# Performance work log

Measured on AMD Instinct MI355X. Metric: run time of the kernel, lower is better.

Reference implementation:

```python
import jax, jax.numpy as jnp
import numpy as np

B, D_IN, H, D_OUT = 1024, 512, 512, 512


def _act(v):
    # torch.relu(x) ** 2
    r = jnp.maximum(v, 0.0)
    return r * r


def setup_inputs() -> dict:
    key = jax.random.key(0)
    ks = jax.random.split(key, 8)
    x = jax.random.normal(ks[0], (B, D_IN), dtype=jnp.float32)
    # input_to_hidden: Linear(D_IN, H)
    W_in = jax.random.normal(ks[1], (D_IN, H), dtype=jnp.float32) / np.sqrt(D_IN)
    b_in = jax.random.normal(ks[2], (H,), dtype=jnp.float32) * 0.01
    # hidden_to_hidden[i]: Linear(1, H-i-1). Pack into padded arrays [H-1, H]
    # where row i, column j is the weight feeding output index j (valid only j > i).
    W_hh = jax.random.normal(ks[3], (H - 1, H), dtype=jnp.float32) * 0.02
    b_hh = jax.random.normal(ks[4], (H - 1, H), dtype=jnp.float32) * 0.01
    # hidden_to_output: Linear(H, D_OUT)
    W_out = jax.random.normal(ks[5], (H, D_OUT), dtype=jnp.float32) / np.sqrt(H)
    b_out = jax.random.normal(ks[6], (D_OUT,), dtype=jnp.float32) * 0.01
    return {"x": x, "W_in": W_in, "b_in": b_in, "W_hh": W_hh, "b_hh": b_hh,
            "W_out": W_out, "b_out": b_out}


def reference(x, W_in, b_in, W_hh, b_hh, W_out, b_out):
    h0 = _act(x @ W_in + b_in)  # [B, H]
    hid = h0.shape[1]
    col = jnp.arange(hid)

    def step(h, inp):
        i, w, b = inp  # w, b: [H] padded rows
        src = jnp.take(h, i, axis=1)  # [B], uses UPDATED h (strict sequential dep)
        contrib = _act(src[:, None] * w[None, :] + b[None, :])  # [B, H]
        mask = (col > i).astype(h.dtype)  # only columns i+1.. get updated
        return h + contrib * mask[None, :], None

    xs = (jnp.arange(hid - 1), W_hh, b_hh)
    h, _ = jax.lax.scan(step, h0, xs)
    return h @ W_out + b_out  # [B, D_OUT]
```

## Files before the change

kernel.cpp:

```cpp
#include <hip/hip_runtime.h>

#define B_SZ 1024
#define DIN 512
#define HH 512
#define DOUT 512

typedef short bf16x8 __attribute__((ext_vector_type(8)));
typedef float f32x4 __attribute__((ext_vector_type(4)));

__device__ __forceinline__ unsigned short f2bf(float f) {
    unsigned int u = __float_as_uint(f);
    u += 0x7FFFu + ((u >> 16) & 1u);
    return (unsigned short)(u >> 16);
}
__device__ __forceinline__ float bf2f(unsigned short s) {
    return __uint_as_float(((unsigned int)s) << 16);
}

__device__ __forceinline__ uint4 cvt8(const float4& a0, const float4& a1, int term) {
    const float av[8] = {a0.x, a0.y, a0.z, a0.w, a1.x, a1.y, a1.z, a1.w};
    unsigned int p[4];
    #pragma unroll
    for (int q = 0; q < 4; ++q) {
        float f0 = av[2 * q], f1 = av[2 * q + 1];
        unsigned short h0 = f2bf(f0), h1 = f2bf(f1);
        if (term == 1) { h0 = f2bf(f0 - bf2f(h0)); h1 = f2bf(f1 - bf2f(h1)); }
        p[q] = (unsigned int)h0 | ((unsigned int)h1 << 16);
    }
    uint4 v; v.x = p[0]; v.y = p[1]; v.z = p[2]; v.w = p[3];
    return v;
}

__device__ __forceinline__ void gload_lds16(const void* g, void* l) {
    __builtin_amdgcn_global_load_lds(
        (__attribute__((address_space(1))) void*)g,
        (__attribute__((address_space(3))) void*)l, 16, 0, 0);
}

template <int N>
__device__ __forceinline__ void waitcnt_vm() {
    asm volatile("s_waitcnt vmcnt(%0)" :: "n"(N) : "memory");
}

__device__ __forceinline__ void convW_body(const float* __restrict__ W,
                                           uint4* __restrict__ dst, int t) {
    const int lane = t & 63;
    const int fb   = t >> 6;
    const int ks   = fb >> 5;
    const int nf   = fb & 31;
    const int col  = nf * 16 + (lane & 15);
    const int kb   = ks * 32 + ((lane >> 4) << 3);
    const int term = kb >> 9;
    const int c0   = kb & 511;
    unsigned short o[8];
    #pragma unroll
    for (int j = 0; j < 8; ++j) {
        const float f = W[(size_t)(c0 + j) * 512 + col];
        unsigned short hi = f2bf(f);
        o[j] = (term == 2) ? f2bf(f - bf2f(hi)) : hi;
    }
    uint4 v;
    v.x = (unsigned int)o[0] | ((unsigned int)o[1] << 16);
    v.y = (unsigned int)o[2] | ((unsigned int)o[3] << 16);
    v.z = (unsigned int)o[4] | ((unsigned int)o[5] << 16);
    v.w = (unsigned int)o[6] | ((unsigned int)o[7] << 16);
    dst[t] = v;
}

template <int C>
__device__ __forceinline__ void pack_bulk(const float* __restrict__ W_hh,
                                          const float* __restrict__ b_hh,
                                          float2* __restrict__ wbk, int e) {
    constexpr int NK = 7 - C;
    constexpr int CB = (C==0?0:C==1?7:C==2?13:C==3?18:C==4?22:C==5?25:27) * 4096;
    const int s   = e / (NK * 64);
    const int rem = e - s * (NK * 64);
    const int row = 64 * C + s;
    const int col = 64 * (C + 1) + rem;
    float2 o;
    o.x = W_hh[(size_t)row * 512 + col];
    o.y = b_hh[(size_t)row * 512 + col];
    wbk[CB + e] = o;
}

__global__ __launch_bounds__(256)
void prep_all(const float* __restrict__ W_hh, const float* __restrict__ b_hh,
              float2* __restrict__ wdg, float2* __restrict__ wbk,
              const float* __restrict__ W_in, uint4* __restrict__ Bin,
              const float* __restrict__ W_out, uint4* __restrict__ Bout) {
    const int b = blockIdx.x;
    const int tid = threadIdx.x;
    if (b < 128) {
        const int idx = b * 256 + tid;
        const int i = idx >> 6, l = idx & 63;
        float2 o;
        if (i < 511 && l > (i & 63)) {
            const int col = ((i >> 6) << 6) + l;
            o.x = W_hh[(size_t)i * 512 + col];
            o.y = b_hh[(size_t)i * 512 + col];
        } else { o.x = 0.0f; o.y = -1.0f; }
        wdg[idx] = o;
    } else if (b < 576) {
        const int rb = b - 128;
        if      (rb < 112) pack_bulk<0>(W_hh, b_hh, wbk, (rb      ) * 256 + tid);
        else if (rb < 208) pack_bulk<1>(W_hh, b_hh, wbk, (rb - 112) * 256 + tid);
        else if (rb < 288) pack_bulk<2>(W_hh, b_hh, wbk, (rb - 208) * 256 + tid);
        else if (rb < 352) pack_bulk<3>(W_hh, b_hh, wbk, (rb - 288) * 256 + tid);
        else if (rb < 400) pack_bulk<4>(W_hh, b_hh, wbk, (rb - 352) * 256 + tid);
        else if (rb < 432) pack_bulk<5>(W_hh, b_hh, wbk, (rb - 400) * 256 + tid);
        else               pack_bulk<6>(W_hh, b_hh, wbk, (rb - 432) * 256 + tid);
    } else if (b < 960) {
        convW_body(W_in, Bin, (b - 576) * 256 + tid);
    } else {
        convW_body(W_out, Bout, (b - 960) * 256 + tid);
    }
}

template <bool ACT>
__global__ __launch_bounds__(512, 2)
void mfma_gemm(const float* __restrict__ A,
               const uint4* __restrict__ Bg,
               const float* __restrict__ bias,
               float* __restrict__ C) {
    __shared__ uint4 lds[2][768];
    const int tid  = threadIdx.x;
    const int lane = tid & 63;
    const int w    = tid >> 6;
    const int mfw  = w & 3;
    const int nfw  = w >> 2;
    const int mf0  = blockIdx.x * 4;
    const int nf0  = blockIdx.y * 2;

    const int ks_s = tid >> 8;
    const int mf_s = (tid >> 6) & 3;
    const int arow = (mf0 + mf_s) * 16 + (lane & 15);
    const int koff = (lane >> 4) << 3;
    const int bks  = tid >> 7;
    const int bnf  = (tid >> 6) & 1;

    float4 Ra0, Ra1; uint4 R2;
    auto stage = [&](int s) {
        const int kp = (s * 2 + ks_s) * 32 + koff;
        const int c  = kp & 511;
        Ra0 = *(const float4*)&A[(size_t)arow * 512 + c];
        Ra1 = *(const float4*)&A[(size_t)arow * 512 + c + 4];
        if (tid < 256)
            R2 = Bg[(size_t)((s * 2 + bks) * 32 + nf0 + bnf) * 64 + lane];
    };
    auto write_tile = [&](int buf, int s) {
        const int kp = (s * 2 + ks_s) * 32 + koff;
        lds[buf][ks_s * 256 + mf_s * 64 + lane] = cvt8(Ra0, Ra1, kp >> 9);
        if (tid < 256)
            lds[buf][512 + bks * 128 + bnf * 64 + lane] = R2;
    };

    f32x4 acc = {0.f, 0.f, 0.f, 0.f};

    stage(0);
    write_tile(0, 0);
    stage(1);
    __syncthreads();

    for (int s = 0; s < 24; ++s) {
        const int cur = s & 1;
        if (s + 1 < 24) write_tile(cur ^ 1, s + 1);
        if (s + 2 < 24) stage(s + 2);
        __builtin_amdgcn_sched_barrier(0);

        bf16x8 aF0 = *(const bf16x8*)&lds[cur][          mfw * 64 + lane];
        bf16x8 aF1 = *(const bf16x8*)&lds[cur][256     + mfw * 64 + lane];
        bf16x8 bF0 = *(const bf16x8*)&lds[cur][512     + nfw * 64 + lane];
        bf16x8 bF1 = *(const bf16x8*)&lds[cur][512+128 + nfw * 64 + lane];
        acc = __builtin_amdgcn_mfma_f32_16x16x32_bf16(aF0, bF0, acc, 0, 0, 0);
        acc = __builtin_amdgcn_mfma_f32_16x16x32_bf16(aF1, bF1, acc, 0, 0, 0);
        __syncthreads();
    }

    const int colg  = (nf0 + nfw) * 16 + (lane & 15);
    const float bv  = bias[colg];
    const int rbase = (mf0 + mfw) * 16 + ((lane >> 4) << 2);
    #pragma unroll
    for (int r = 0; r < 4; ++r) {
        float v = acc[r] + bv;
        if (ACT) { v = fmaxf(v, 0.f); v = v * v; }
        C[(size_t)(rbase + r) * 512 + colg] = v;
    }
}

template <int C>
__device__ __forceinline__ void scan_chunk(const float2* __restrict__ wdg,
                                           const float2* __restrict__ wbk,
                                           float2 (* __restrict__ smb)[3584],
                                           float hr[8], int lane, int tid) {
    constexpr int NK = 7 - C;
    constexpr int CB = (C==0?0:C==1?7:C==2?13:C==3?18:C==4?22:C==5?25:C==6?27:27) * 4096;
    const float2* dptr = wdg + (64 * C) * 64 + lane;

    const char* gch = (const char*)(wbk + CB);
    char* lbase = (char*)(&smb[0][0]) + ((tid >> 6) << 10);
    auto stage = [&](int t, int buf) {
        const char* g = gch + (size_t)t * (NK * 4096);
        char* l = lbase + buf * 28672;
        #pragma unroll
        for (int u = 0; u < NK; ++u)
            gload_lds16(g + (size_t)((u << 8) + tid) * 16, l + (u << 12));
    };
    if constexpr (NK > 0) { stage(0, 0); stage(1, 1); }
    __builtin_amdgcn_sched_barrier(0);

    float2 Wd[16];
    #pragma unroll
    for (int q = 0; q < 16; ++q) Wd[q] = dptr[q * 64];

    for (int t = 0; t < 4; ++t) {
        #pragma unroll
        for (int q = 0; q < 16; ++q) {
            const int s = t * 16 + q;
            if (!(C == 7 && s == 63)) {
                const float hi = __uint_as_float(
                    __builtin_amdgcn_readlane(__float_as_uint(hr[C]), s));
                const float tv = fmaf(hi, Wd[q].x, Wd[q].y);
                const float rv = fmaxf(tv, 0.f);
                hr[C] = fmaf(rv, rv, hr[C]);
            }
            if (t < 3) Wd[q] = dptr[(s + 16) * 64];
        }
    }

    if constexpr (NK > 0) {
        #pragma unroll
        for (int t = 0; t < 8; ++t) {
            if (t + 2 < 8) stage(t + 2, (t + 2) & 3);
            __builtin_amdgcn_sched_barrier(0);
            if      (t <= 5) waitcnt_vm<2 * NK>();
            else if (t == 6) waitcnt_vm<NK>();
            else             waitcnt_vm<0>();
            __builtin_amdgcn_s_barrier();
            __builtin_amdgcn_sched_barrier(0);

            #pragma unroll 2
            for (int s = 0; s < 8; ++s) {
                const float hi = __uint_as_float(
                    __builtin_amdgcn_readlane(__float_as_uint(hr[C]), t * 8 + s));
                #pragma unroll
                for (int k = 0; k < NK; ++k) {
                    const float2 wv = smb[t & 3][(s * NK + k) * 64 + lane];
                    const float tv = fmaf(hi, wv.x, wv.y);
                    const float rv = fmaxf(tv, 0.f);
                    hr[C + 1 + k] = fmaf(rv, rv, hr[C + 1 + k]);
                }
            }
        }
    }
}

__global__ __launch_bounds__(256, 1)
void scan_kernel(const float2* __restrict__ wdg, const float2* __restrict__ wbk,
                 float* __restrict__ h) {
    __shared__ __align__(16) float2 smb[4][3584];
    const int tid  = threadIdx.x;
    const int lane = tid & 63;
    const int wave = tid >> 6;
    const int row  = blockIdx.x * 4 + wave;
    float* hrow = h + (size_t)row * HH;

    float hr[8];
    #pragma unroll
    for (int k = 0; k < 8; ++k) hr[k] = hrow[lane + 64 * k];

    scan_chunk<0>(wdg, wbk, smb, hr, lane, tid);
    scan_chunk<1>(wdg, wbk, smb, hr, lane, tid);
    scan_chunk<2>(wdg, wbk, smb, hr, lane, tid);
    scan_chunk<3>(wdg, wbk, smb, hr, lane, tid);
    scan_chunk<4>(wdg, wbk, smb, hr, lane, tid);
    scan_chunk<5>(wdg, wbk, smb, hr, lane, tid);
    scan_chunk<6>(wdg, wbk, smb, hr, lane, tid);
    scan_chunk<7>(wdg, wbk, smb, hr, lane, tid);

    #pragma unroll
    for (int k = 0; k < 8; ++k) hrow[lane + 64 * k] = hr[k];
}

extern "C" void kernel_launch(void* const* d_in, const int* in_sizes, int n_in,
                              void* d_out, int out_size, void* d_ws, size_t ws_size,
                              hipStream_t stream) {
    const float* x     = (const float*)d_in[0];
    const float* W_in  = (const float*)d_in[1];
    const float* b_in  = (const float*)d_in[2];
    const float* W_hh  = (const float*)d_in[3];
    const float* b_hh  = (const float*)d_in[4];
    const float* W_out = (const float*)d_in[5];
    const float* b_out = (const float*)d_in[6];
    float* out = (float*)d_out;

    char* ws = (char*)d_ws;
    float2* wdg  = (float2*)ws;
    float2* wbk  = (float2*)(ws + 0x040000u);
    float*  h    = (float*)(ws + 0x120000u);
    uint4*  Bin  = (uint4*)(ws + 0x320000u);
    uint4*  Bout = (uint4*)(ws + 0x4A0000u);

    prep_all<<<dim3(1344), dim3(256), 0, stream>>>(W_hh, b_hh, wdg, wbk,
                                                   W_in, Bin, W_out, Bout);

    mfma_gemm<true><<<dim3(16, 16), dim3(512), 0, stream>>>(x, Bin, b_in, h);

    scan_kernel<<<dim3(256), dim3(256), 0, stream>>>(wdg, wbk, h);

    mfma_gemm<false><<<dim3(16, 16), dim3(512), 0, stream>>>(h, Bout, b_out, out);
}
```

Measured before the change: 160.5 us.

## Split each scan row across two waves sharing hidden columns via LDS

The scan kernel now uses 512 threads per block, so each batch row is handled by two waves that own interleaved 64-column chunks of the hidden state. The wave owning the current diagonal chunk runs the sequential inner scan and publishes its chunk through a small shared buffer. Both waves then apply the bulk updates for their own columns, which halves per-wave register state and bulk work and doubles wave count. The cost is an extra block-wide barrier per chunk, plus the non-owner wave sitting idle during the serial diagonal phase.

```diff
diff --git a/kernel.cpp b/kernel.cpp
--- a/kernel.cpp
+++ b/kernel.cpp
@@ -187,14 +187,35 @@
     }
 }
 
+template <int C, int H>
+__device__ __forceinline__ void bulk_half(const float2* __restrict__ tile,
+                                          const float his[8], float hrl[4],
+                                          int lane) {
+    constexpr int NK = 7 - C;
+    constexpr int I0 = (C + 2 - H) >> 1;
+    #pragma unroll
+    for (int s = 0; s < 8; ++s) {
+        #pragma unroll
+        for (int i = I0; i < 4; ++i) {
+            const float2 wv = tile[(s * NK + (2 * i + H - C - 1)) * 64 + lane];
+            const float tv = fmaf(his[s], wv.x, wv.y);
+            const float rv = fmaxf(tv, 0.f);
+            hrl[i] = fmaf(rv, rv, hrl[i]);
+        }
+    }
+}
+
 template <int C>
 __device__ __forceinline__ void scan_chunk(const float2* __restrict__ wdg,
                                            const float2* __restrict__ wbk,
                                            float2 (* __restrict__ smb)[3584],
-                                           float hr[8], int lane, int tid) {
+                                           float (* __restrict__ comm)[64],
+                                           float hrl[4], int lane, int half,
+                                           int r, int tid) {
     constexpr int NK = 7 - C;
     constexpr int CB = (C==0?0:C==1?7:C==2?13:C==3?18:C==4?22:C==5?25:C==6?27:27) * 4096;
-    const float2* dptr = wdg + (64 * C) * 64 + lane;
+    constexpr int IO = C >> 1;
+    const bool owner = (half == (C & 1));
 
     const char* gch = (const char*)(wbk + CB);
     char* lbase = (char*)(&smb[0][0]) + ((tid >> 6) << 10);
@@ -205,32 +226,40 @@
         for (int u = 0; u < NK; ++u)
             gload_lds16(g + (size_t)((u << 8) + tid) * 16, l + (u << 12));
     };
-    if constexpr (NK > 0) { stage(0, 0); stage(1, 1); }
+    if constexpr (NK > 0) {
+        if (tid < 256) { stage(0, 0); stage(1, 1); }
+    }
     __builtin_amdgcn_sched_barrier(0);
 
-    float2 Wd[16];
-    #pragma unroll
-    for (int q = 0; q < 16; ++q) Wd[q] = dptr[q * 64];
-
-    for (int t = 0; t < 4; ++t) {
+    if (owner) {
+        const float2* dptr = wdg + (64 * C) * 64 + lane;
+        float2 Wd[16];
         #pragma unroll
-        for (int q = 0; q < 16; ++q) {
-            const int s = t * 16 + q;
-            if (!(C == 7 && s == 63)) {
-                const float hi = __uint_as_float(
-                    __builtin_amdgcn_readlane(__float_as_uint(hr[C]), s));
-                const float tv = fmaf(hi, Wd[q].x, Wd[q].y);
-                const float rv = fmaxf(tv, 0.f);
-                hr[C] = fmaf(rv, rv, hr[C]);
+        for (int q = 0; q < 16; ++q) Wd[q] = dptr[q * 64];
+        for (int t = 0; t < 4; ++t) {
+            #pragma unroll
+            for (int q = 0; q < 16; ++q) {
+                const int s = t * 16 + q;
+                if (!(C == 7 && s == 63)) {
+                    const float hi = __uint_as_float(
+                        __builtin_amdgcn_readlane(__float_as_uint(hrl[IO]), s));
+                    const float tv = fmaf(hi, Wd[q].x, Wd[q].y);
+                    const float rv = fmaxf(tv, 0.f);
+                    hrl[IO] = fmaf(rv, rv, hrl[IO]);
+                }
+                if (t < 3) Wd[q] = dptr[(s + 16) * 64];
             }
-            if (t < 3) Wd[q] = dptr[(s + 16) * 64];
         }
     }
 
     if constexpr (NK > 0) {
+        if (owner) comm[r][lane] = hrl[IO];
+        __syncthreads();
+        const float hsrc = owner ? hrl[IO] : comm[r][lane];
+
         #pragma unroll
         for (int t = 0; t < 8; ++t) {
-            if (t + 2 < 8) stage(t + 2, (t + 2) & 3);
+            if (tid < 256 && t + 2 < 8) stage(t + 2, (t + 2) & 3);
             __builtin_amdgcn_sched_barrier(0);
             if      (t <= 5) waitcnt_vm<2 * NK>();
             else if (t == 6) waitcnt_vm<NK>();
@@ -238,47 +267,44 @@
             __builtin_amdgcn_s_barrier();
             __builtin_amdgcn_sched_barrier(0);
 
-            #pragma unroll 2
-            for (int s = 0; s < 8; ++s) {
-                const float hi = __uint_as_float(
-                    __builtin_amdgcn_readlane(__float_as_uint(hr[C]), t * 8 + s));
-                #pragma unroll
-                for (int k = 0; k < NK; ++k) {
-                    const float2 wv = smb[t & 3][(s * NK + k) * 64 + lane];
-                    const float tv = fmaf(hi, wv.x, wv.y);
-                    const float rv = fmaxf(tv, 0.f);
-                    hr[C + 1 + k] = fmaf(rv, rv, hr[C + 1 + k]);
-                }
-            }
+            float his[8];
+            #pragma unroll
+            for (int s = 0; s < 8; ++s)
+                his[s] = __uint_as_float(__builtin_amdgcn_readlane(
+                    __float_as_uint(hsrc), t * 8 + s));
+            if (half == 0) bulk_half<C, 0>(&smb[t & 3][0], his, hrl, lane);
+            else           bulk_half<C, 1>(&smb[t & 3][0], his, hrl, lane);
         }
     }
 }
 
-__global__ __launch_bounds__(256, 1)
+__global__ __launch_bounds__(512, 2)
 void scan_kernel(const float2* __restrict__ wdg, const float2* __restrict__ wbk,
                  float* __restrict__ h) {
     __shared__ __align__(16) float2 smb[4][3584];
+    __shared__ float comm[4][64];
     const int tid  = threadIdx.x;
     const int lane = tid & 63;
-    const int wave = tid >> 6;
-    const int row  = blockIdx.x * 4 + wave;
-    float* hrow = h + (size_t)row * HH;
-
-    float hr[8];
-    #pragma unroll
-    for (int k = 0; k < 8; ++k) hr[k] = hrow[lane + 64 * k];
-
-    scan_chunk<0>(wdg, wbk, smb, hr, lane, tid);
-    scan_chunk<1>(wdg, wbk, smb, hr, lane, tid);
-    scan_chunk<2>(wdg, wbk, smb, hr, lane, tid);
-    scan_chunk<3>(wdg, wbk, smb, hr, lane, tid);
-    scan_chunk<4>(wdg, wbk, smb, hr, lane, tid);
-    scan_chunk<5>(wdg, wbk, smb, hr, lane, tid);
-    scan_chunk<6>(wdg, wbk, smb, hr, lane, tid);
-    scan_chunk<7>(wdg, wbk, smb, hr, lane, tid);
-
-    #pragma unroll
-    for (int k = 0; k < 8; ++k) hrow[lane + 64 * k] = hr[k];
+    const int w    = tid >> 6;
+    const int r    = w & 3;
+    const int half = w >> 2;
+    float* hrow = h + (size_t)(blockIdx.x * 4 + r) * HH;
+
+    float hrl[4];
+    #pragma unroll
+    for (int i = 0; i < 4; ++i) hrl[i] = hrow[lane + 64 * (2 * i + half)];
+
+    scan_chunk<0>(wdg, wbk, smb, comm, hrl, lane, half, r, tid);
+    scan_chunk<1>(wdg, wbk, smb, comm, hrl, lane, half, r, tid);
+    scan_chunk<2>(wdg, wbk, smb, comm, hrl, lane, half, r, tid);
+    scan_chunk<3>(wdg, wbk, smb, comm, hrl, lane, half, r, tid);
+    scan_chunk<4>(wdg, wbk, smb, comm, hrl, lane, half, r, tid);
+    scan_chunk<5>(wdg, wbk, smb, comm, hrl, lane, half, r, tid);
+    scan_chunk<6>(wdg, wbk, smb, comm, hrl, lane, half, r, tid);
+    scan_chunk<7>(wdg, wbk, smb, comm, hrl, lane, half, r, tid);
+
+    #pragma unroll
+    for (int i = 0; i < 4; ++i) hrow[lane + 64 * (2 * i + half)] = hrl[i];
 }
 
 extern "C" void kernel_launch(void* const* d_in, const int* in_sizes, int n_in,
@@ -305,7 +331,7 @@
 
     mfma_gemm<true><<<dim3(16, 16), dim3(512), 0, stream>>>(x, Bin, b_in, h);
 
-    scan_kernel<<<dim3(256), dim3(256), 0, stream>>>(wdg, wbk, h);
+    scan_kernel<<<dim3(256), dim3(512), 0, stream>>>(wdg, wbk, h);
 
     mfma_gemm<false><<<dim3(16, 16), dim3(512), 0, stream>>>(h, Bout, b_out, out);
 }
```

After: 188.3 us. 17.4% more time.
